# Performance work log

Measured on AMD Instinct MI355X. Metric: run time of the kernel, lower is better.

Reference implementation:

```python
import jax, jax.numpy as jnp
import numpy as np

D = 300        # emb_dim
G = 2000       # number of graphs in the batch
NEG_TORCH = 0.01  # torch F.leaky_relu default slope (GATEConv / lin1)
NEG_GAT = 0.2     # PyG GATConv negative_slope


def seg_softmax(a, idx, n):
    m = jax.ops.segment_max(a, idx, num_segments=n)
    e = jnp.exp(a - m[idx])
    s = jax.ops.segment_sum(e, idx, num_segments=n)
    return e / (s[idx] + 1e-16)


def gru_cell(inp, h, wih, whh, bih, bhh):
    gi = inp @ wih.T + bih
    gh = h @ whh.T + bhh
    ir, iz, in_ = jnp.split(gi, 3, axis=-1)
    hr, hz, hn = jnp.split(gh, 3, axis=-1)
    r = jax.nn.sigmoid(ir + hr)
    z = jax.nn.sigmoid(iz + hz)
    n = jnp.tanh(in_ + r * hn)
    return (1.0 - z) * n + z * h


def setup_inputs():
    key = jax.random.key(0)
    ks = iter(jax.random.split(key, 64))
    N, E = 50000, 200000
    nrm = lambda *s: 0.1 * jax.random.normal(next(ks), s, dtype=jnp.float32)
    return dict(
        x=jax.random.randint(next(ks), (N, 2), 0, 3),
        edge_index=jax.random.randint(next(ks), (2, E), 0, N),
        edge_attr=jax.random.randint(next(ks), (E, 2), 0, 3),
        batch=jnp.sort(jax.random.randint(next(ks), (N,), 0, G)),
        emb_atom=nrm(120, D), emb_chir=nrm(3, D),
        lin1_W=nrm(D, D), lin1_b=nrm(D),
        ge_e1=nrm(6, D), ge_e2=nrm(3, D),
        ge_att_l=nrm(D), ge_att_r=nrm(D),
        ge_lin1_W=nrm(D, 2 * D), ge_lin2_W=nrm(D, D), ge_bias=nrm(D),
        gat_W=nrm(4, D, D), gat_att_s=nrm(4, D), gat_att_d=nrm(4, D), gat_b=nrm(4, D),
        gru_wih=nrm(5, 3 * D, D), gru_whh=nrm(5, 3 * D, D),
        gru_bih=nrm(5, 3 * D), gru_bhh=nrm(5, 3 * D),
        mol_Ws=nrm(D, D), mol_Wd=nrm(D, D),
        mol_att_s=nrm(D), mol_att_d=nrm(D), mol_b=nrm(D),
        mgru_wih=nrm(3 * D, D), mgru_whh=nrm(3 * D, D),
        mgru_bih=nrm(3 * D), mgru_bhh=nrm(3 * D),
        lin2_W=nrm(1, D), lin2_b=nrm(1),
    )


def reference(x, edge_index, edge_attr, batch,
              emb_atom, emb_chir, lin1_W, lin1_b,
              ge_e1, ge_e2, ge_att_l, ge_att_r, ge_lin1_W, ge_lin2_W, ge_bias,
              gat_W, gat_att_s, gat_att_d, gat_b,
              gru_wih, gru_whh, gru_bih, gru_bhh,
              mol_Ws, mol_Wd, mol_att_s, mol_att_d, mol_b,
              mgru_wih, mgru_whh, mgru_bih, mgru_bhh,
              lin2_W, lin2_b):
    N = x.shape[0]
    xf = emb_atom[x[:, 0]] + emb_chir[x[:, 1]]
    xf = jax.nn.leaky_relu(xf @ lin1_W.T + lin1_b, NEG_TORCH)

    # --- layer 0: GATEConv (with self-loops, edge embeddings) ---
    loop = jnp.arange(N)
    src = jnp.concatenate([edge_index[0], loop])
    dst = jnp.concatenate([edge_index[1], loop])
    bt = jnp.concatenate([edge_attr[:, 0], jnp.full((N,), 4, edge_attr.dtype)])
    bd = jnp.concatenate([edge_attr[:, 1], jnp.zeros((N,), edge_attr.dtype)])
    eemb = ge_e1[bt] + ge_e2[bd]                                   # [E+N, D]
    xj = jax.nn.leaky_relu(
        jnp.concatenate([xf[src], eemb], axis=-1) @ ge_lin1_W.T, NEG_TORCH)
    alpha = jax.nn.leaky_relu(xj @ ge_att_l + xf[dst] @ ge_att_r, NEG_TORCH)
    alpha = seg_softmax(alpha, dst, N)
    h = jax.ops.segment_sum((xj @ ge_lin2_W.T) * alpha[:, None], dst,
                            num_segments=N) + ge_bias
    xf = jax.nn.relu(gru_cell(jax.nn.elu(h), xf,
                              gru_wih[0], gru_whh[0], gru_bih[0], gru_bhh[0]))

    # --- layers 1..4: GATConv (heads=1, add_self_loops=False) ---
    s, d = edge_index[0], edge_index[1]
    for l in range(4):
        xw = xf @ gat_W[l].T
        alpha = jax.nn.leaky_relu((xw @ gat_att_s[l])[s] + (xw @ gat_att_d[l])[d],
                                  NEG_GAT)
        alpha = seg_softmax(alpha, d, N)
        h = jax.ops.segment_sum(xw[s] * alpha[:, None], d,
                                num_segments=N) + gat_b[l]
        xf = jax.nn.relu(gru_cell(jax.nn.elu(h), xf, gru_wih[l + 1],
                                  gru_whh[l + 1], gru_bih[l + 1], gru_bhh[l + 1]))

    # --- attentive readout: bipartite GATConv atoms -> molecules ---
    out = jax.nn.relu(jax.ops.segment_sum(xf, batch, num_segments=G))
    for _ in range(3):
        xs = xf @ mol_Ws.T
        xd = out @ mol_Wd.T
        alpha = jax.nn.leaky_relu(xs @ mol_att_s + (xd @ mol_att_d)[batch], NEG_GAT)
        alpha = seg_softmax(alpha, batch, G)
        h = jax.ops.segment_sum(xs * alpha[:, None], batch, num_segments=G) + mol_b
        out = jax.nn.relu(gru_cell(jax.nn.elu(h), out,
                                   mgru_wih, mgru_whh, mgru_bih, mgru_bhh))

    pred = out @ lin2_W.T + lin2_b
    return (out, pred)
```

## Files before the change

### kernel.cpp

```cpp
#include <hip/hip_runtime.h>

constexpr int D = 300;
constexpr int KP = 320;

static inline int cdiv(int a, int b){ return (a + b - 1) / b; }

__device__ __forceinline__ unsigned short f2bf(float f){
  unsigned u = __float_as_uint(f);
  unsigned r = (u + 0x7fffu + ((u >> 16) & 1u)) >> 16;
  return (unsigned short)r;
}
__device__ __forceinline__ float bf2f(unsigned short h){
  return __uint_as_float((unsigned)h << 16);
}
__device__ __forceinline__ float pread(const unsigned short* __restrict__ h,
                                       const unsigned short* __restrict__ l, size_t i){
  return bf2f(h[i]) + bf2f(l[i]);
}
__device__ __forceinline__ void pwrite(unsigned short* __restrict__ h,
                                       unsigned short* __restrict__ l, size_t i, float v){
  unsigned short hi = f2bf(v);
  h[i] = hi; l[i] = f2bf(v - bf2f(hi));
}
__device__ __forceinline__ int xcd_chunk(int bid, int nwg){
  int q = nwg >> 3, r = nwg & 7;
  int x = bid & 7, i = bid >> 3;
  return (x < r ? x * (q + 1) : r * (q + 1) + (x - r) * q) + i;
}

typedef __attribute__((ext_vector_type(8))) short bf16x8;
typedef __attribute__((ext_vector_type(4))) float f32x4;
typedef unsigned short us;

__global__ void k_cvt2(const float* __restrict__ src, int ld, int M,
                       us* __restrict__ hb, us* __restrict__ lb, int total){
  int idx = blockIdx.x * blockDim.x + threadIdx.x;
  if (idx >= total) return;
  int r = idx / 80, k4 = (idx - r * 80) * 4;
  const float* row = src + (size_t)r * ld;
  bool rm = r < M;
  ushort4 oh, ol;
  float x;
  x = (rm && k4 + 0 < D) ? row[k4 + 0] : 0.f; oh.x = f2bf(x); ol.x = f2bf(x - bf2f(oh.x));
  x = (rm && k4 + 1 < D) ? row[k4 + 1] : 0.f; oh.y = f2bf(x); ol.y = f2bf(x - bf2f(oh.y));
  x = (rm && k4 + 2 < D) ? row[k4 + 2] : 0.f; oh.z = f2bf(x); ol.z = f2bf(x - bf2f(oh.z));
  x = (rm && k4 + 3 < D) ? row[k4 + 3] : 0.f; oh.w = f2bf(x); ol.w = f2bf(x - bf2f(oh.w));
  *(ushort4*)(hb + (size_t)r * KP + k4) = oh;
  *(ushort4*)(lb + (size_t)r * KP + k4) = ol;
}

__global__ void k_wpack(const float* __restrict__ Wih, const float* __restrict__ Whh,
                        us* __restrict__ out){
  int idx = blockIdx.x * blockDim.x + threadIdx.x;
  if (idx >= 307200) return;
  int h4 = idx * 4;
  int jtks = h4 / 12288;
  int within = h4 - jtks * 12288;
  int jt = jtks / 10, ks = jtks - (jtks / 10) * 10;
  int t = within >> 10;
  int w2 = within & 1023;
  int kg = w2 >> 8;
  int row = (w2 >> 3) & 31;
  int h0 = w2 & 7;
  int m = t / 6, g = (t >> 1) % 3, p = t & 1;
  int j = jt * 32 + row;
  const float* W = m ? Whh : Wih;
  ushort4 o;
  us* po = (us*)&o;
  #pragma unroll
  for (int u = 0; u < 4; ++u){
    int k = ks * 32 + kg * 8 + h0 + u;
    float v = (j < D && k < D) ? W[(size_t)(g * D + j) * D + k] : 0.f;
    us hi = f2bf(v);
    po[u] = p ? f2bf(v - bf2f(hi)) : hi;
  }
  *(ushort4*)(out + h4) = o;
}

template<int MODE>
__global__ void k_mfma3(const us* __restrict__ Ah, const us* __restrict__ Al,
                        const us* __restrict__ Bh, const us* __restrict__ Bl,
                        const float* __restrict__ bias,
                        us* __restrict__ Ch, us* __restrict__ Cl,
                        int M, int NC){
  __shared__ short ls[4][4096];
  const int tid = threadIdx.x;
  const int lane = tid & 63;
  const int wid = tid >> 6, wr = wid >> 1, wc = wid & 1;
  int work = xcd_chunk(blockIdx.x, gridDim.x);
  const int rowBase = (work / 3) * 128, colBase = (work - (work / 3) * 3) * 128;
  const int l15 = lane & 15, l4 = lane >> 4;
  f32x4 acc[4][4] = {};
  const us* gsrc[4] = {Ah, Al, Bh, Bl};

  for (int k0 = 0; k0 < KP; k0 += 32){
    #pragma unroll
    for (int t = 0; t < 4; ++t){
      int base = (t < 2) ? rowBase : colBase;
      #pragma unroll
      for (int s = 0; s < 2; ++s){
        int lin = s * 256 + tid;
        int kg = lin >> 7, row = lin & 127;
        const us* g = gsrc[t] + (size_t)(base + row) * KP + k0 + kg * 8;
        short* lb = &ls[t][0] + (size_t)(s * 256 + (tid & ~63)) * 8;
        __builtin_amdgcn_global_load_lds((const __attribute__((address_space(1))) unsigned*)g,
                                         (__attribute__((address_space(3))) unsigned*)lb, 16, 0, 0);
      }
    }
    __syncthreads();
    bf16x8 fbh[4], fbl[4];
    #pragma unroll
    for (int j = 0; j < 4; ++j){
      int bi = l4 * 128 + wc * 64 + j * 16 + l15;
      fbh[j] = *(const bf16x8*)(&ls[2][0] + (size_t)bi * 8);
      fbl[j] = *(const bf16x8*)(&ls[3][0] + (size_t)bi * 8);
    }
    #pragma unroll
    for (int i = 0; i < 4; ++i){
      int ai = l4 * 128 + wr * 64 + i * 16 + l15;
      bf16x8 fah = *(const bf16x8*)(&ls[0][0] + (size_t)ai * 8);
      bf16x8 fal = *(const bf16x8*)(&ls[1][0] + (size_t)ai * 8);
      #pragma unroll
      for (int j = 0; j < 4; ++j){
        acc[i][j] = __builtin_amdgcn_mfma_f32_16x16x32_bf16(fah, fbh[j], acc[i][j], 0, 0, 0);
        acc[i][j] = __builtin_amdgcn_mfma_f32_16x16x32_bf16(fah, fbl[j], acc[i][j], 0, 0, 0);
        acc[i][j] = __builtin_amdgcn_mfma_f32_16x16x32_bf16(fal, fbh[j], acc[i][j], 0, 0, 0);
      }
    }
    __syncthreads();
  }

  #pragma unroll
  for (int i = 0; i < 4; ++i){
    #pragma unroll
    for (int q = 0; q < 4; ++q){
      int r = rowBase + wr * 64 + i * 16 + l4 * 4 + q;
      if (r >= M) continue;
      #pragma unroll
      for (int j = 0; j < 4; ++j){
        int c = colBase + wc * 64 + j * 16 + l15;
        if (c >= KP) continue;
        size_t o = (size_t)r * KP + c;
        if (c >= NC){ Ch[o] = 0; Cl[o] = 0; continue; }
        float v = acc[i][j][q];
        if (MODE) v += bias[c];
        if (MODE == 1) v = v > 0.f ? v : 0.01f * v;
        if (MODE == 2) v = v > 0.f ? v : (expf(v) - 1.f);
        pwrite(Ch, Cl, o, v);
      }
    }
  }
}

__global__ __launch_bounds__(256, 2) void k_gru(
    const us* __restrict__ Ih, const us* __restrict__ Il,
    const us* __restrict__ Hh, const us* __restrict__ Hl,
    const us* __restrict__ Wp,
    const float* __restrict__ bih, const float* __restrict__ bhh,
    us* __restrict__ Oh, us* __restrict__ Ol){
  __shared__ short lsW[2][12288];
  const int tid = threadIdx.x, lane = tid & 63, wid = tid >> 6;
  const int l15 = lane & 15, l4 = lane >> 4;
  int work = xcd_chunk(blockIdx.x, gridDim.x);
  const int rt = work / 10, jt = work - rt * 10;
  const int rowBase = rt * 128;
  f32x4 acc[2][2][6] = {};
  const us* asrc[4] = {Ih, Il, Hh, Hl};
  bf16x8 fa[2][2][4];

  auto loadA = [&](int ks, int buf){
    int k0 = ks * 32;
    #pragma unroll
    for (int r = 0; r < 2; ++r){
      size_t base = (size_t)(rowBase + wid * 32 + r * 16 + l15) * KP + k0 + l4 * 8;
      #pragma unroll
      for (int t = 0; t < 4; ++t)
        fa[buf][r][t] = *(const bf16x8*)(asrc[t] + base);
    }
  };
  auto stageW = [&](int ks, int buf){
    const us* wsrc = Wp + (size_t)(jt * 10 + ks) * 12288;
    #pragma unroll
    for (int s = 0; s < 6; ++s){
      int lin = s * 256 + tid;
      __builtin_amdgcn_global_load_lds(
        (const __attribute__((address_space(1))) unsigned*)(wsrc + (size_t)lin * 8),
        (__attribute__((address_space(3))) unsigned*)(&lsW[buf][0] + (size_t)(s * 256 + (tid & ~63)) * 8),
        16, 0, 0);
    }
  };
  auto compute = [&](int buf){
    #pragma unroll
    for (int c = 0; c < 2; ++c){
      #pragma unroll
      for (int mg = 0; mg < 6; ++mg){
        const int m = mg / 3, g = mg % 3, tH = m * 6 + g * 2;
        int wro = c * 16 + l15;
        bf16x8 wh = *(const bf16x8*)(&lsW[buf][0] + (size_t)((tH * 4 + l4) * 32 + wro) * 8);
        bf16x8 wl = *(const bf16x8*)(&lsW[buf][0] + (size_t)(((tH + 1) * 4 + l4) * 32 + wro) * 8);
        #pragma unroll
        for (int r = 0; r < 2; ++r){
          acc[r][c][mg] = __builtin_amdgcn_mfma_f32_16x16x32_bf16(fa[buf][r][m*2],   wh, acc[r][c][mg], 0, 0, 0);
          acc[r][c][mg] = __builtin_amdgcn_mfma_f32_16x16x32_bf16(fa[buf][r][m*2],   wl, acc[r][c][mg], 0, 0, 0);
          acc[r][c][mg] = __builtin_amdgcn_mfma_f32_16x16x32_bf16(fa[buf][r][m*2+1], wh, acc[r][c][mg], 0, 0, 0);
        }
      }
    }
  };

  loadA(0, 0); stageW(0, 0);
  __syncthreads();
  for (int ks2 = 0; ks2 < 5; ++ks2){
    int ks = ks2 * 2;
    if (ks < 9){ loadA(ks + 1, 1); stageW(ks + 1, 1); }
    compute(0);
    __syncthreads();
    if (ks + 2 <= 9){ loadA(ks + 2, 0); stageW(ks + 2, 0); }
    compute(1);
    __syncthreads();
  }

  #pragma unroll
  for (int c = 0; c < 2; ++c){
    int j = jt * 32 + c * 16 + l15;
    bool jok = j < D;
    float b0=0.f,b1=0.f,b2=0.f,c0=0.f,c1=0.f,c2=0.f;
    if (jok){ b0=bih[j]; b1=bih[j+300]; b2=bih[j+600]; c0=bhh[j]; c1=bhh[j+300]; c2=bhh[j+600]; }
    #pragma unroll
    for (int r = 0; r < 2; ++r){
      #pragma unroll
      for (int q = 0; q < 4; ++q){
        int row = rowBase + wid * 32 + r * 16 + l4 * 4 + q;
        float o = 0.f;
        if (jok){
          float ir = acc[r][c][0][q] + b0, iz = acc[r][c][1][q] + b1, in_ = acc[r][c][2][q] + b2;
          float hr = acc[r][c][3][q] + c0, hz = acc[r][c][4][q] + c1, hn  = acc[r][c][5][q] + c2;
          float rg = 1.f / (1.f + expf(-(ir + hr)));
          float zg = 1.f / (1.f + expf(-(iz + hz)));
          float nn = tanhf(in_ + rg * hn);
          float h = pread(Hh, Hl, (size_t)row * KP + j);
          o = (1.f - zg) * nn + zg * h;
          o = o > 0.f ? o : 0.f;
        }
        if (j < KP) pwrite(Oh, Ol, (size_t)row * KP + j, o);
      }
    }
  }
}

__global__ void k_embed2(const int* __restrict__ x, const float* __restrict__ ea,
                         const float* __restrict__ ec, us* __restrict__ hb,
                         us* __restrict__ lb, int N, int total){
  int idx = blockIdx.x * blockDim.x + threadIdx.x;
  if (idx >= total) return;
  int r = idx / KP, j = idx - r * KP;
  float v = (r < N && j < D) ? ea[x[2*r] * D + j] + ec[x[2*r+1] * D + j] : 0.f;
  pwrite(hb, lb, idx, v);
}

__global__ void k_table(const float* __restrict__ e1, const float* __restrict__ e2,
                        const float* __restrict__ W1, float* __restrict__ T){
  int c = blockIdx.x, t = c / 3, d = c - 3 * (c / 3);
  __shared__ float se[D];
  for (int k = threadIdx.x; k < D; k += blockDim.x) se[k] = e1[t*D + k] + e2[d*D + k];
  __syncthreads();
  for (int j = threadIdx.x; j < KP; j += blockDim.x){
    float s = 0.f;
    if (j < D) for (int k = 0; k < D; ++k) s += se[k] * W1[(size_t)j * 600 + 300 + k];
    T[c * KP + j] = s;
  }
}

__global__ void k_pads(const float* __restrict__ ge_att_l, const float* __restrict__ ge_att_r,
                       const float* __restrict__ gat_att_s, const float* __restrict__ gat_att_d,
                       const float* __restrict__ mol_att_s, const float* __restrict__ mol_att_d,
                       const float* __restrict__ gat_b, const float* __restrict__ mol_b,
                       const float* __restrict__ lin2_W, float* __restrict__ vp){
  int idx = blockIdx.x * blockDim.x + threadIdx.x;
  if (idx >= 18 * KP) return;
  int s = idx / KP, j = idx - s * KP;
  float v = 0.f;
  if (j < D){
    if (s == 0) v = ge_att_l[j];
    else if (s == 1) v = ge_att_r[j];
    else if (s < 6)  v = gat_att_s[(s - 2) * D + j];
    else if (s < 10) v = gat_att_d[(s - 6) * D + j];
    else if (s == 10) v = mol_att_s[j];
    else if (s == 11) v = mol_att_d[j];
    else if (s < 16) v = gat_b[(s - 12) * D + j];
    else if (s == 16) v = mol_b[j];
    else v = lin2_W[j];
  }
  vp[idx] = v;
}

__device__ __forceinline__ void load8f(const float* __restrict__ p, float* v){
  float4 a = *(const float4*)p, b = *(const float4*)(p + 4);
  v[0]=a.x; v[1]=a.y; v[2]=a.z; v[3]=a.w; v[4]=b.x; v[5]=b.y; v[6]=b.z; v[7]=b.w;
}
__device__ __forceinline__ void store8p(us* __restrict__ h, us* __restrict__ l,
                                        size_t ob, const float* v){
  ushort4 h0, h1, l0, l1;
  #pragma unroll
  for (int u = 0; u < 8; ++u){
    us hi = f2bf(v[u]), lo = f2bf(v[u] - bf2f(hi));
    if (u < 4){ ((us*)&h0)[u] = hi; ((us*)&l0)[u] = lo; }
    else      { ((us*)&h1)[u-4] = hi; ((us*)&l1)[u-4] = lo; }
  }
  *(ushort4*)(h + ob) = h0; *(ushort4*)(h + ob + 4) = h1;
  *(ushort4*)(l + ob) = l0; *(ushort4*)(l + ob + 4) = l1;
}

__global__ void k_dot2(const us* __restrict__ Ahp, const us* __restrict__ Alp,
                       const float* __restrict__ vp, float* __restrict__ out, int M){
  int w = (blockIdx.x * blockDim.x + threadIdx.x) >> 6;
  int lane = threadIdx.x & 63;
  if (w >= M) return;
  float s = 0.f;
  if (lane < 40){
    int jb = lane * 8;
    size_t b = (size_t)w * KP + jb;
    bf16x8 hv = *(const bf16x8*)(Ahp + b), lv = *(const bf16x8*)(Alp + b);
    float vv[8]; load8f(vp + jb, vv);
    #pragma unroll
    for (int u = 0; u < 8; ++u) s += (bf2f((us)hv[u]) + bf2f((us)lv[u])) * vv[u];
  }
  #pragma unroll
  for (int o = 32; o; o >>= 1) s += __shfl_xor(s, o);
  if (lane == 0) out[w] = s;
}

__global__ void k_hist(const int* __restrict__ ei, int E, int* __restrict__ hist){
  int e = blockIdx.x * blockDim.x + threadIdx.x;
  if (e < E) atomicAdd(&hist[ei[E + e]], 1);
}
template<int BS>
__global__ void k_scanA(const int* __restrict__ in, int* __restrict__ out,
                        int* __restrict__ bsum, int n){
  __shared__ int s[BS];
  int t = threadIdx.x, gid = blockIdx.x * BS + t;
  int v = (gid < n) ? in[gid] : 0;
  s[t] = v; __syncthreads();
  for (int o = 1; o < BS; o <<= 1){
    int add = (t >= o) ? s[t - o] : 0;
    __syncthreads();
    s[t] += add;
    __syncthreads();
  }
  if (gid < n) out[gid] = s[t] - v;
  if (t == BS - 1) bsum[blockIdx.x] = s[BS - 1];
}
template<int BS>
__global__ void k_scanB(int* __restrict__ bsum, int nb){
  __shared__ int s[BS];
  int t = threadIdx.x;
  int v = (t < nb) ? bsum[t] : 0;
  s[t] = v; __syncthreads();
  for (int o = 1; o < BS; o <<= 1){
    int add = (t >= o) ? s[t - o] : 0;
    __syncthreads();
    s[t] += add;
    __syncthreads();
  }
  if (t < nb) bsum[t] = s[t] - v;
}
template<int BS>
__global__ void k_scanC(int* __restrict__ out, const int* __restrict__ bsum, int n){
  int gid = blockIdx.x * BS + threadIdx.x;
  if (gid < n) out[gid] += bsum[blockIdx.x];
}
__global__ void k_setN(int* __restrict__ off, int N, int E){ off[N] = E; }
__global__ void k_fill(const int* __restrict__ ei, int E, const int* __restrict__ off,
                       int* __restrict__ cnt, int* __restrict__ lst){
  int e = blockIdx.x * blockDim.x + threadIdx.x;
  if (e >= E) return;
  int d = ei[E + e];
  int p = off[d] + atomicAdd(&cnt[d], 1);
  lst[p] = e;
}
__global__ void k_goff(const int* __restrict__ batch, int N, int G, int* __restrict__ goff){
  int g = blockIdx.x * blockDim.x + threadIdx.x;
  if (g > G) return;
  int lo = 0, hi = N;
  while (lo < hi){ int mid = (lo + hi) >> 1; if (batch[mid] < g) lo = mid + 1; else hi = mid; }
  goff[g] = lo;
}

__global__ void k_gate_fused(const us* __restrict__ uh, const us* __restrict__ ul,
                             const float* __restrict__ Tp, const float* __restrict__ att_lp,
                             const float* __restrict__ rvec,
                             const int* __restrict__ ei, const int* __restrict__ ea,
                             const int* __restrict__ off, const int* __restrict__ lst,
                             us* __restrict__ oh, us* __restrict__ ol, int N){
  int d = (blockIdx.x * blockDim.x + threadIdx.x) >> 6;
  int lane = threadIdx.x & 63;
  if (d >= N) return;
  bool act = lane < 40;
  int jb = lane * 8;
  float al[8] = {};
  if (act) load8f(att_lp + jb, al);
  int beg = off[d], deg = off[d + 1] - beg;
  float rd = rvec[d];
  float accv[8] = {}, m = -1e30f, s = 0.f;
  for (int ii = 0; ii <= deg; ++ii){
    int src, c;
    if (ii < deg){ int e = lst[beg + ii]; src = ei[e]; c = ea[2*e] * 3 + ea[2*e + 1]; }
    else { src = d; c = 12; }
    float xv[8] = {}; float part = 0.f;
    if (act){
      size_t ub = (size_t)src * KP + jb;
      bf16x8 hv = *(const bf16x8*)(uh + ub), lv = *(const bf16x8*)(ul + ub);
      float tv[8]; load8f(Tp + c * KP + jb, tv);
      #pragma unroll
      for (int u = 0; u < 8; ++u){
        float v = bf2f((us)hv[u]) + bf2f((us)lv[u]) + tv[u];
        v = v > 0.f ? v : 0.01f * v;
        part += v * al[u];
        xv[u] = v;
      }
    }
    #pragma unroll
    for (int o = 32; o; o >>= 1) part += __shfl_xor(part, o);
    float l = part + rd; l = l > 0.f ? l : 0.01f * l;
    float mn = fmaxf(m, l);
    float sc = expf(m - mn), p = expf(l - mn);
    #pragma unroll
    for (int u = 0; u < 8; ++u) accv[u] = accv[u] * sc + p * xv[u];
    s = s * sc + p; m = mn;
  }
  if (act){
    float inv = 1.f / (s + 1e-16f);
    float v[8];
    #pragma unroll
    for (int u = 0; u < 8; ++u) v[u] = accv[u] * inv;
    store8p(oh, ol, (size_t)d * KP + jb, v);
  }
}

__global__ void k_gat_fused(const us* __restrict__ xh, const us* __restrict__ xl,
                            const float* __restrict__ as_, const float* __restrict__ ad,
                            const int* __restrict__ ei,
                            const int* __restrict__ off, const int* __restrict__ lst,
                            const float* __restrict__ biasp,
                            us* __restrict__ oh, us* __restrict__ ol, int N){
  int d = (blockIdx.x * blockDim.x + threadIdx.x) >> 6;
  int lane = threadIdx.x & 63;
  if (d >= N) return;
  bool act = lane < 40;
  int jb = lane * 8;
  int beg = off[d], deg = off[d + 1] - beg;
  float add = ad[d];
  float accv[8] = {}, m = -1e30f, s = 0.f;
  for (int ii = 0; ii < deg; ++ii){
    int e = lst[beg + ii];
    int src = ei[e];
    float l = as_[src] + add; l = l > 0.f ? l : 0.2f * l;
    float mn = fmaxf(m, l);
    float sc = expf(m - mn), p = expf(l - mn);
    if (act){
      size_t ub = (size_t)src * KP + jb;
      bf16x8 hv = *(const bf16x8*)(xh + ub), lv = *(const bf16x8*)(xl + ub);
      #pragma unroll
      for (int u = 0; u < 8; ++u)
        accv[u] = accv[u] * sc + p * (bf2f((us)hv[u]) + bf2f((us)lv[u]));
    }
    s = s * sc + p; m = mn;
  }
  if (act){
    float inv = 1.f / (s + 1e-16f);
    float bv[8]; load8f(biasp + jb, bv);
    float v[8];
    #pragma unroll
    for (int u = 0; u < 8; ++u){
      float w = accv[u] * inv + bv[u];
      v[u] = w > 0.f ? w : (expf(w) - 1.f);
    }
    store8p(oh, ol, (size_t)d * KP + jb, v);
  }
}

__global__ void k_mol_fused(const us* __restrict__ xh, const us* __restrict__ xl,
                            const float* __restrict__ asx, const float* __restrict__ adg,
                            const int* __restrict__ goff, const float* __restrict__ biasp,
                            us* __restrict__ oh, us* __restrict__ ol, int G){
  int g = (blockIdx.x * blockDim.x + threadIdx.x) >> 6;
  int lane = threadIdx.x & 63;
  if (g >= G) return;
  bool act = lane < 40;
  int jb = lane * 8;
  int beg = goff[g], end = goff[g + 1];
  float add = adg[g];
  float accv[8] = {}, m = -1e30f, s = 0.f;
  for (int i = beg; i < end; ++i){
    float l = asx[i] + add; l = l > 0.f ? l : 0.2f * l;
    float mn = fmaxf(m, l);
    float sc = expf(m - mn), p = expf(l - mn);
    if (act){
      size_t ub = (size_t)i * KP + jb;
      bf16x8 hv = *(const bf16x8*)(xh + ub), lv = *(const bf16x8*)(xl + ub);
      #pragma unroll
      for (int u = 0; u < 8; ++u)
        accv[u] = accv[u] * sc + p * (bf2f((us)hv[u]) + bf2f((us)lv[u]));
    }
    s = s * sc + p; m = mn;
  }
  if (act){
    float inv = 1.f / (s + 1e-16f);
    float bv[8]; load8f(biasp + jb, bv);
    float v[8];
    #pragma unroll
    for (int u = 0; u < 8; ++u){
      float w = accv[u] * inv + bv[u];
      v[u] = w > 0.f ? w : (expf(w) - 1.f);
    }
    store8p(oh, ol, (size_t)g * KP + jb, v);
  }
}

__global__ void k_gsum(const us* __restrict__ xh, const us* __restrict__ xl,
                       const int* __restrict__ goff,
                       us* __restrict__ oh, us* __restrict__ ol, int G){
  int g = (blockIdx.x * blockDim.x + threadIdx.x) >> 6;
  int lane = threadIdx.x & 63;
  if (g >= G) return;
  bool act = lane < 40;
  int jb = lane * 8;
  int beg = goff[g], end = goff[g + 1];
  float a[8] = {};
  if (act){
    for (int i = beg; i < end; ++i){
      size_t ub = (size_t)i * KP + jb;
      bf16x8 hv = *(const bf16x8*)(xh + ub), lv = *(const bf16x8*)(xl + ub);
      #pragma unroll
      for (int u = 0; u < 8; ++u) a[u] += bf2f((us)hv[u]) + bf2f((us)lv[u]);
    }
    float v[8];
    #pragma unroll
    for (int u = 0; u < 8; ++u) v[u] = fmaxf(a[u], 0.f);
    store8p(oh, ol, (size_t)g * KP + jb, v);
  }
}

__global__ void k_final2(const us* __restrict__ Oh, const us* __restrict__ Ol,
                         const float* __restrict__ w2p, const float* __restrict__ b2,
                         float* __restrict__ out, int G){
  int g = (blockIdx.x * blockDim.x + threadIdx.x) >> 6;
  int lane = threadIdx.x & 63;
  if (g >= G) return;
  float s = 0.f;
  if (lane < 40){
    int jb = lane * 8;
    size_t b = (size_t)g * KP + jb;
    bf16x8 hv = *(const bf16x8*)(Oh + b), lv = *(const bf16x8*)(Ol + b);
    float wv[8]; load8f(w2p + jb, wv);
    #pragma unroll
    for (int u = 0; u < 8; ++u){
      float v = bf2f((us)hv[u]) + bf2f((us)lv[u]);
      if (jb + u < D) out[(size_t)g * D + jb + u] = v;
      s += v * wv[u];
    }
  }
  #pragma unroll
  for (int o = 32; o; o >>= 1) s += __shfl_xor(s, o);
  if (lane == 0) out[(size_t)G * D + g] = s + b2[0];
}

extern "C" void kernel_launch(void* const* d_in, const int* in_sizes, int n_in,
                              void* d_out, int out_size, void* d_ws, size_t ws_size,
                              hipStream_t stream){
  (void)n_in; (void)ws_size;
  const int*   x         = (const int*)d_in[0];
  const int*   ei        = (const int*)d_in[1];
  const int*   ea        = (const int*)d_in[2];
  const int*   batch     = (const int*)d_in[3];
  const float* emb_atom  = (const float*)d_in[4];
  const float* emb_chir  = (const float*)d_in[5];
  const float* lin1_W    = (const float*)d_in[6];
  const float* lin1_b    = (const float*)d_in[7];
  const float* ge_e1     = (const float*)d_in[8];
  const float* ge_e2     = (const float*)d_in[9];
  const float* ge_att_l  = (const float*)d_in[10];
  const float* ge_att_r  = (const float*)d_in[11];
  const float* ge_lin1_W = (const float*)d_in[12];
  const float* ge_lin2_W = (const float*)d_in[13];
  const float* ge_bias   = (const float*)d_in[14];
  const float* gat_W     = (const float*)d_in[15];
  const float* gat_att_s = (const float*)d_in[16];
  const float* gat_att_d = (const float*)d_in[17];
  const float* gat_b     = (const float*)d_in[18];
  const float* gru_wih   = (const float*)d_in[19];
  const float* gru_whh   = (const float*)d_in[20];
  const float* gru_bih   = (const float*)d_in[21];
  const float* gru_bhh   = (const float*)d_in[22];
  const float* mol_Ws    = (const float*)d_in[23];
  const float* mol_Wd    = (const float*)d_in[24];
  const float* mol_att_s = (const float*)d_in[25];
  const float* mol_att_d = (const float*)d_in[26];
  const float* mol_b     = (const float*)d_in[27];
  const float* mgru_wih  = (const float*)d_in[28];
  const float* mgru_whh  = (const float*)d_in[29];
  const float* mgru_bih  = (const float*)d_in[30];
  const float* mgru_bhh  = (const float*)d_in[31];
  const float* lin2_W    = (const float*)d_in[32];
  const float* lin2_b    = (const float*)d_in[33];

  const int N  = in_sizes[0] / 2;
  const int E  = in_sizes[1] / 2;
  const int G  = out_size / (D + 1);
  const int Npad = cdiv(N, 128) * 128;
  const int Gpad = cdiv(G, 128) * 128;

  char* base = (char*)d_ws;
  size_t used = 0;
  auto alloc = [&](size_t bytes) -> void* {
    void* p = base + used;
    used += (bytes + 255) & ~(size_t)255;
    return p;
  };
  us* PaH = (us*)alloc((size_t)Npad * KP * 2); us* PaL = (us*)alloc((size_t)Npad * KP * 2);
  us* PbH = (us*)alloc((size_t)Npad * KP * 2); us* PbL = (us*)alloc((size_t)Npad * KP * 2);
  us* PcH = (us*)alloc((size_t)Npad * KP * 2); us* PcL = (us*)alloc((size_t)Npad * KP * 2);
  us* QaH = (us*)alloc((size_t)Gpad * KP * 2); us* QaL = (us*)alloc((size_t)Gpad * KP * 2);
  us* QbH = (us*)alloc((size_t)Gpad * KP * 2); us* QbL = (us*)alloc((size_t)Gpad * KP * 2);
  us* QcH = (us*)alloc((size_t)Gpad * KP * 2); us* QcL = (us*)alloc((size_t)Gpad * KP * 2);
  auto wsm = [&](void){ return (us*)alloc((size_t)384 * KP * 2); };
  us *wlin1H=wsm(), *wlin1L=wsm(), *wgeuH=wsm(), *wgeuL=wsm(), *wge2H=wsm(), *wge2L=wsm();
  us *wgatH[4], *wgatL[4];
  for (int l = 0; l < 4; ++l){ wgatH[l]=wsm(); wgatL[l]=wsm(); }
  us *wmolSH=wsm(), *wmolSL=wsm(), *wmolDH=wsm(), *wmolDL=wsm();
  us* Wgru[6];
  for (int l = 0; l < 6; ++l) Wgru[l] = (us*)alloc((size_t)1228800 * 2);
  float* Tt  = (float*)alloc((size_t)18 * KP * 4);
  float* vp  = (float*)alloc((size_t)18 * KP * 4);
  float* rv  = (float*)alloc((size_t)N * 4);
  float* adv = (float*)alloc((size_t)N * 4);
  float* asx = (float*)alloc((size_t)N * 4);
  const int SBS = 512;
  int nblk = cdiv(N, SBS);
  int* hist = (int*)alloc((size_t)N * 4);
  int* cnt  = (int*)alloc((size_t)N * 4);
  int* off  = (int*)alloc((size_t)(N + 1) * 4);
  int* bsum = (int*)alloc((size_t)nblk * 4);
  int* lst  = (int*)alloc((size_t)E * 4);
  int* goff = (int*)alloc((size_t)(G + 1) * 4);

  auto cvt2 = [&](const float* src, int ld, int M, us* hb, us* lb, int Mpad){
    int tot = Mpad * 80;
    k_cvt2<<<cdiv(tot, 256), 256, 0, stream>>>(src, ld, M, hb, lb, tot);
  };
  auto mm_p = [&](const us* ah, const us* al, const us* bh, const us* bl,
                  const float* bias, us* ch, us* cl, int M, int NC, int mode){
    int nwg = cdiv(M, 128) * 3;
    if (mode == 0)      k_mfma3<0><<<nwg, 256, 0, stream>>>(ah, al, bh, bl, bias, ch, cl, M, NC);
    else if (mode == 1) k_mfma3<1><<<nwg, 256, 0, stream>>>(ah, al, bh, bl, bias, ch, cl, M, NC);
    else                k_mfma3<2><<<nwg, 256, 0, stream>>>(ah, al, bh, bl, bias, ch, cl, M, NC);
  };
  auto gru = [&](const us* Ih, const us* Il, const us* Hh, const us* Hl,
                 const us* Wp, const float* bi, const float* bh,
                 us* Oh, us* Ol, int Mpad){
    int nwg = (Mpad / 128) * 10;
    k_gru<<<nwg, 256, 0, stream>>>(Ih, Il, Hh, Hl, Wp, bi, bh, Oh, Ol);
  };

  hipMemsetAsync(hist, 0, (size_t)N * 4, stream);
  k_hist<<<cdiv(E, 256), 256, 0, stream>>>(ei, E, hist);
  k_scanA<SBS><<<nblk, SBS, 0, stream>>>(hist, off, bsum, N);
  k_scanB<SBS><<<1, SBS, 0, stream>>>(bsum, nblk);
  k_scanC<SBS><<<nblk, SBS, 0, stream>>>(off, bsum, N);
  k_setN<<<1, 1, 0, stream>>>(off, N, E);
  hipMemsetAsync(cnt, 0, (size_t)N * 4, stream);
  k_fill<<<cdiv(E, 256), 256, 0, stream>>>(ei, E, off, cnt, lst);
  k_goff<<<cdiv(G + 1, 256), 256, 0, stream>>>(batch, N, G, goff);

  cvt2(lin1_W, D, D, wlin1H, wlin1L, 384);
  cvt2(ge_lin1_W, 2 * D, D, wgeuH, wgeuL, 384);
  cvt2(ge_lin2_W, D, D, wge2H, wge2L, 384);
  for (int l = 0; l < 4; ++l) cvt2(gat_W + (size_t)l * D * D, D, D, wgatH[l], wgatL[l], 384);
  cvt2(mol_Ws, D, D, wmolSH, wmolSL, 384);
  cvt2(mol_Wd, D, D, wmolDH, wmolDL, 384);
  for (int l = 0; l < 5; ++l)
    k_wpack<<<1200, 256, 0, stream>>>(gru_wih + (size_t)l * 270000,
                                      gru_whh + (size_t)l * 270000, Wgru[l]);
  k_wpack<<<1200, 256, 0, stream>>>(mgru_wih, mgru_whh, Wgru[5]);
  k_table<<<18, 256, 0, stream>>>(ge_e1, ge_e2, ge_lin1_W, Tt);
  k_pads<<<cdiv(18 * KP, 256), 256, 0, stream>>>(ge_att_l, ge_att_r, gat_att_s, gat_att_d,
                                                 mol_att_s, mol_att_d, gat_b, mol_b, lin2_W, vp);

  k_embed2<<<cdiv(Npad * KP, 256), 256, 0, stream>>>(x, emb_atom, emb_chir, PaH, PaL, N, Npad * KP);
  mm_p(PaH, PaL, wlin1H, wlin1L, lin1_b, PbH, PbL, N, D, 1);

  mm_p(PbH, PbL, wgeuH, wgeuL, nullptr, PaH, PaL, N, D, 0);
  k_dot2<<<cdiv(N, 4), 256, 0, stream>>>(PbH, PbL, vp + 1 * KP, rv, N);
  k_gate_fused<<<cdiv(N, 4), 256, 0, stream>>>(PaH, PaL, Tt, vp, rv,
                                               ei, ea, off, lst, PcH, PcL, N);
  mm_p(PcH, PcL, wge2H, wge2L, ge_bias, PaH, PaL, N, D, 2);
  gru(PaH, PaL, PbH, PbL, Wgru[0], gru_bih, gru_bhh, PcH, PcL, Npad);

  us *xfH = PcH, *xfL = PcL, *aH = PaH, *aL = PaL, *bH = PbH, *bL = PbL;
  for (int l = 0; l < 4; ++l){
    mm_p(xfH, xfL, wgatH[l], wgatL[l], nullptr, aH, aL, N, D, 0);
    k_dot2<<<cdiv(N, 4), 256, 0, stream>>>(aH, aL, vp + (2 + l) * KP, rv, N);
    k_dot2<<<cdiv(N, 4), 256, 0, stream>>>(aH, aL, vp + (6 + l) * KP, adv, N);
    k_gat_fused<<<cdiv(N, 4), 256, 0, stream>>>(aH, aL, rv, adv, ei, off, lst,
                                                vp + (12 + l) * KP, bH, bL, N);
    gru(bH, bL, xfH, xfL, Wgru[l + 1],
        gru_bih + (l + 1) * 900, gru_bhh + (l + 1) * 900, aH, aL, Npad);
    us* th = xfH; us* tl = xfL;
    xfH = aH; xfL = aL; aH = th; aL = tl;
  }

  k_gsum<<<cdiv(G, 4), 256, 0, stream>>>(xfH, xfL, goff, QaH, QaL, G);
  mm_p(xfH, xfL, wmolSH, wmolSL, nullptr, aH, aL, N, D, 0);
  k_dot2<<<cdiv(N, 4), 256, 0, stream>>>(aH, aL, vp + 10 * KP, asx, N);
  us *outH = QaH, *outL = QaL, *sgH = QbH, *sgL = QbL, *xdH = QcH, *xdL = QcL;
  for (int t = 0; t < 3; ++t){
    mm_p(outH, outL, wmolDH, wmolDL, nullptr, xdH, xdL, G, D, 0);
    k_dot2<<<cdiv(G, 4), 256, 0, stream>>>(xdH, xdL, vp + 11 * KP, adv, G);
    k_mol_fused<<<cdiv(G, 4), 256, 0, stream>>>(aH, aL, asx, adv, goff,
                                                vp + 16 * KP, sgH, sgL, G);
    gru(sgH, sgL, outH, outL, Wgru[5], mgru_bih, mgru_bhh, xdH, xdL, Gpad);
    us* th = outH; us* tl = outL;
    outH = xdH; outL = xdL; xdH = th; xdL = tl;
  }
  k_final2<<<cdiv(G, 4), 256, 0, stream>>>(outH, outL, vp + 17 * KP, lin2_b, (float*)d_out, G);
}
```

Before: 2.858 ms.

## Double-buffer LDS staging with explicit vmcnt waits in MFMA GEMM kernels

The split-bf16 MFMA GEMM kernel now double-buffers its LDS tiles, issuing the next k-slice's global_load_lds before computing the current one. Partial s_waitcnt vmcnt plus raw s_barrier with sched_barrier fences replace the __syncthreads calls. The fused GRU GEMM kernel gets the same explicit vmcnt/barrier scheme with the W staging reordered ahead of the A loads. The aim is to hide global-load latency behind MFMA work. In exchange it doubles LDS use, which may lower occupancy, and the correctness of the hand-picked vmcnt counts depends on exact instruction ordering.

```diff
diff --git a/kernel.cpp b/kernel.cpp
--- a/kernel.cpp
+++ b/kernel.cpp
@@ -26,6 +26,11 @@
   int q = nwg >> 3, r = nwg & 7;
   int x = bid & 7, i = bid >> 3;
   return (x < r ? x * (q + 1) : r * (q + 1) + (x - r) * q) + i;
+}
+__device__ __forceinline__ void barx(){
+  __builtin_amdgcn_sched_barrier(0);
+  __builtin_amdgcn_s_barrier();
+  __builtin_amdgcn_sched_barrier(0);
 }
 
 typedef __attribute__((ext_vector_type(8))) short bf16x8;
@@ -83,7 +88,7 @@
                         const float* __restrict__ bias,
                         us* __restrict__ Ch, us* __restrict__ Cl,
                         int M, int NC){
-  __shared__ short ls[4][4096];
+  __shared__ short ls[2][4][4096];
   const int tid = threadIdx.x;
   const int lane = tid & 63;
   const int wid = tid >> 6, wr = wid >> 1, wc = wid & 1;
@@ -93,7 +98,7 @@
   f32x4 acc[4][4] = {};
   const us* gsrc[4] = {Ah, Al, Bh, Bl};
 
-  for (int k0 = 0; k0 < KP; k0 += 32){
+  auto stage = [&](int k0, int buf){
     #pragma unroll
     for (int t = 0; t < 4; ++t){
       int base = (t < 2) ? rowBase : colBase;
@@ -102,24 +107,25 @@
         int lin = s * 256 + tid;
         int kg = lin >> 7, row = lin & 127;
         const us* g = gsrc[t] + (size_t)(base + row) * KP + k0 + kg * 8;
-        short* lb = &ls[t][0] + (size_t)(s * 256 + (tid & ~63)) * 8;
+        short* lb = &ls[buf][t][0] + (size_t)(s * 256 + (tid & ~63)) * 8;
         __builtin_amdgcn_global_load_lds((const __attribute__((address_space(1))) unsigned*)g,
                                          (__attribute__((address_space(3))) unsigned*)lb, 16, 0, 0);
       }
     }
-    __syncthreads();
+  };
+  auto compute = [&](int buf){
     bf16x8 fbh[4], fbl[4];
     #pragma unroll
     for (int j = 0; j < 4; ++j){
       int bi = l4 * 128 + wc * 64 + j * 16 + l15;
-      fbh[j] = *(const bf16x8*)(&ls[2][0] + (size_t)bi * 8);
-      fbl[j] = *(const bf16x8*)(&ls[3][0] + (size_t)bi * 8);
+      fbh[j] = *(const bf16x8*)(&ls[buf][2][0] + (size_t)bi * 8);
+      fbl[j] = *(const bf16x8*)(&ls[buf][3][0] + (size_t)bi * 8);
     }
     #pragma unroll
     for (int i = 0; i < 4; ++i){
       int ai = l4 * 128 + wr * 64 + i * 16 + l15;
-      bf16x8 fah = *(const bf16x8*)(&ls[0][0] + (size_t)ai * 8);
-      bf16x8 fal = *(const bf16x8*)(&ls[1][0] + (size_t)ai * 8);
+      bf16x8 fah = *(const bf16x8*)(&ls[buf][0][0] + (size_t)ai * 8);
+      bf16x8 fal = *(const bf16x8*)(&ls[buf][1][0] + (size_t)ai * 8);
       #pragma unroll
       for (int j = 0; j < 4; ++j){
         acc[i][j] = __builtin_amdgcn_mfma_f32_16x16x32_bf16(fah, fbh[j], acc[i][j], 0, 0, 0);
@@ -127,7 +133,25 @@
         acc[i][j] = __builtin_amdgcn_mfma_f32_16x16x32_bf16(fal, fbh[j], acc[i][j], 0, 0, 0);
       }
     }
-    __syncthreads();
+  };
+
+  stage(0, 0);
+  for (int kk = 0; kk < 5; ++kk){
+    int k0 = kk * 64;
+    stage(k0 + 32, 1);
+    asm volatile("s_waitcnt vmcnt(8)" ::: "memory");
+    barx();
+    compute(0);
+    barx();
+    if (kk < 4){
+      stage(k0 + 64, 0);
+      asm volatile("s_waitcnt vmcnt(8)" ::: "memory");
+    } else {
+      asm volatile("s_waitcnt vmcnt(0)" ::: "memory");
+    }
+    barx();
+    compute(1);
+    barx();
   }
 
   #pragma unroll
@@ -208,16 +232,23 @@
     }
   };
 
-  loadA(0, 0); stageW(0, 0);
-  __syncthreads();
+  stageW(0, 0); loadA(0, 0);
   for (int ks2 = 0; ks2 < 5; ++ks2){
     int ks = ks2 * 2;
-    if (ks < 9){ loadA(ks + 1, 1); stageW(ks + 1, 1); }
+    stageW(ks + 1, 1); loadA(ks + 1, 1);
+    asm volatile("s_waitcnt vmcnt(14)" ::: "memory");
+    barx();
     compute(0);
-    __syncthreads();
-    if (ks + 2 <= 9){ loadA(ks + 2, 0); stageW(ks + 2, 0); }
+    barx();
+    if (ks2 < 4){
+      stageW(ks + 2, 0); loadA(ks + 2, 0);
+      asm volatile("s_waitcnt vmcnt(14)" ::: "memory");
+    } else {
+      asm volatile("s_waitcnt vmcnt(0)" ::: "memory");
+    }
+    barx();
     compute(1);
-    __syncthreads();
+    barx();
   }
 
   #pragma unroll
```

Result: slower. 3.187 ms (+11.5%).

## Remove double buffering from GRU GEMM kernel to cut LDS and register use

Applied to the files above, without the earlier changes.

Replaces the double-buffered LDS weight staging and register A-fragment prefetch in k_gru with a single buffer that is loaded, synchronized, then consumed. It also drops the min-blocks hint in launch_bounds. The aim is lower LDS and VGPR pressure, which could raise occupancy. In exchange, global loads no longer overlap with MFMA compute inside a block, so latency has to be hidden by other resident blocks.

```diff
diff --git a/kernel.cpp b/kernel.cpp
--- a/kernel.cpp
+++ b/kernel.cpp
@@ -152,13 +152,13 @@
   }
 }
 
-__global__ __launch_bounds__(256, 2) void k_gru(
+__global__ __launch_bounds__(256) void k_gru(
     const us* __restrict__ Ih, const us* __restrict__ Il,
     const us* __restrict__ Hh, const us* __restrict__ Hl,
     const us* __restrict__ Wp,
     const float* __restrict__ bih, const float* __restrict__ bhh,
     us* __restrict__ Oh, us* __restrict__ Ol){
-  __shared__ short lsW[2][12288];
+  __shared__ short lsW[12288];
   const int tid = threadIdx.x, lane = tid & 63, wid = tid >> 6;
   const int l15 = lane & 15, l4 = lane >> 4;
   int work = xcd_chunk(blockIdx.x, gridDim.x);
@@ -166,58 +166,54 @@
   const int rowBase = rt * 128;
   f32x4 acc[2][2][6] = {};
   const us* asrc[4] = {Ih, Il, Hh, Hl};
-  bf16x8 fa[2][2][4];
-
-  auto loadA = [&](int ks, int buf){
+  bf16x8 fa[2][4];
+
+  auto loadA = [&](int ks){
     int k0 = ks * 32;
     #pragma unroll
     for (int r = 0; r < 2; ++r){
       size_t base = (size_t)(rowBase + wid * 32 + r * 16 + l15) * KP + k0 + l4 * 8;
       #pragma unroll
       for (int t = 0; t < 4; ++t)
-        fa[buf][r][t] = *(const bf16x8*)(asrc[t] + base);
+        fa[r][t] = *(const bf16x8*)(asrc[t] + base);
     }
   };
-  auto stageW = [&](int ks, int buf){
+  auto stageW = [&](int ks){
     const us* wsrc = Wp + (size_t)(jt * 10 + ks) * 12288;
     #pragma unroll
     for (int s = 0; s < 6; ++s){
       int lin = s * 256 + tid;
       __builtin_amdgcn_global_load_lds(
         (const __attribute__((address_space(1))) unsigned*)(wsrc + (size_t)lin * 8),
-        (__attribute__((address_space(3))) unsigned*)(&lsW[buf][0] + (size_t)(s * 256 + (tid & ~63)) * 8),
+        (__attribute__((address_space(3))) unsigned*)(&lsW[0] + (size_t)(s * 256 + (tid & ~63)) * 8),
         16, 0, 0);
     }
   };
-  auto compute = [&](int buf){
+  auto compute = [&](){
     #pragma unroll
     for (int c = 0; c < 2; ++c){
       #pragma unroll
       for (int mg = 0; mg < 6; ++mg){
         const int m = mg / 3, g = mg % 3, tH = m * 6 + g * 2;
         int wro = c * 16 + l15;
-        bf16x8 wh = *(const bf16x8*)(&lsW[buf][0] + (size_t)((tH * 4 + l4) * 32 + wro) * 8);
-        bf16x8 wl = *(const bf16x8*)(&lsW[buf][0] + (size_t)(((tH + 1) * 4 + l4) * 32 + wro) * 8);
+        bf16x8 wh = *(const bf16x8*)(&lsW[0] + (size_t)((tH * 4 + l4) * 32 + wro) * 8);
+        bf16x8 wl = *(const bf16x8*)(&lsW[0] + (size_t)(((tH + 1) * 4 + l4) * 32 + wro) * 8);
         #pragma unroll
         for (int r = 0; r < 2; ++r){
-          acc[r][c][mg] = __builtin_amdgcn_mfma_f32_16x16x32_bf16(fa[buf][r][m*2],   wh, acc[r][c][mg], 0, 0, 0);
-          acc[r][c][mg] = __builtin_amdgcn_mfma_f32_16x16x32_bf16(fa[buf][r][m*2],   wl, acc[r][c][mg], 0, 0, 0);
-          acc[r][c][mg] = __builtin_amdgcn_mfma_f32_16x16x32_bf16(fa[buf][r][m*2+1], wh, acc[r][c][mg], 0, 0, 0);
+          acc[r][c][mg] = __builtin_amdgcn_mfma_f32_16x16x32_bf16(fa[r][m*2],   wh, acc[r][c][mg], 0, 0, 0);
+          acc[r][c][mg] = __builtin_amdgcn_mfma_f32_16x16x32_bf16(fa[r][m*2],   wl, acc[r][c][mg], 0, 0, 0);
+          acc[r][c][mg] = __builtin_amdgcn_mfma_f32_16x16x32_bf16(fa[r][m*2+1], wh, acc[r][c][mg], 0, 0, 0);
         }
       }
     }
   };
 
-  loadA(0, 0); stageW(0, 0);
-  __syncthreads();
-  for (int ks2 = 0; ks2 < 5; ++ks2){
-    int ks = ks2 * 2;
-    if (ks < 9){ loadA(ks + 1, 1); stageW(ks + 1, 1); }
-    compute(0);
+  stageW(0); loadA(0);
+  for (int ks = 0; ks < 10; ++ks){
     __syncthreads();
-    if (ks + 2 <= 9){ loadA(ks + 2, 0); stageW(ks + 2, 0); }
-    compute(1);
+    compute();
     __syncthreads();
+    if (ks < 9){ stageW(ks + 1); loadA(ks + 1); }
   }
 
   #pragma unroll
```

Result: slower. 3.588 ms (+25.5%).
